# Kernel optimization log

Measured on AMD Instinct MI355X. Metric: run time of the kernel, lower is better.

## Reference

```python
import jax, jax.numpy as jnp
import numpy as np

INPUT_DIM = 1024
CODEBOOK_DIM = 128
CODEBOOK_SIZE = 8192
B, N = 8, 4096


def setup_inputs() -> dict:
    key = jax.random.key(0)
    k1, k2, k3 = jax.random.split(key, 3)
    x = jax.random.normal(k1, (B, N, INPUT_DIM), dtype=jnp.float32)
    # xavier_normal_: std = sqrt(2 / (fan_in + fan_out))
    xavier_std = float(np.sqrt(2.0 / (INPUT_DIM + CODEBOOK_DIM)))
    random_projection = jax.random.normal(k2, (INPUT_DIM, CODEBOOK_DIM), dtype=jnp.float32) * xavier_std
    codebook = jax.random.normal(k3, (CODEBOOK_SIZE, CODEBOOK_DIM), dtype=jnp.float32)
    return {"x": x, "random_projection": random_projection, "codebook": codebook}


def reference(x, random_projection, codebook):
    # random projection: [B, N, D] @ [D, E] -> [B, N, E]
    proj = jnp.einsum("bnd,de->bne", x, random_projection)
    b, n, e = proj.shape
    flat = proj.reshape(b * n, e)  # [BN, E]
    eps = 1e-12  # matches torch F.normalize default eps
    nx = flat / jnp.maximum(jnp.linalg.norm(flat, axis=1, keepdims=True), eps)
    ncb = codebook / jnp.maximum(jnp.linalg.norm(codebook, axis=1, keepdims=True), eps)
    # squared euclidean distances [K, BN]; argmin of d^2 == argmin of cdist
    d2 = (
        jnp.sum(ncb * ncb, axis=1)[:, None]
        + jnp.sum(nx * nx, axis=1)[None, :]
        - 2.0 * (ncb @ nx.T)
    )
    nearest = jnp.argmin(d2, axis=0)  # [BN]
    return nearest.reshape(b, n).astype(jnp.int32)
```

## Files before the change

### kernel.cpp

```cpp
#include <hip/hip_runtime.h>
#include <math.h>
#include <float.h>
#include <limits.h>

#define BN      32768
#define D_IN    1024
#define E_DIM   128
#define CB_N    8192

typedef _Float16 f16x8 __attribute__((ext_vector_type(8)));
typedef _Float16 f16x4 __attribute__((ext_vector_type(4)));
typedef float    f32x4 __attribute__((ext_vector_type(4)));


__global__ __launch_bounds__(256) void pack_all_kernel(
    const float* __restrict__ cb, _Float16* __restrict__ ph,
    _Float16* __restrict__ pl,
    const float* __restrict__ rp, _Float16* __restrict__ rph,
    _Float16* __restrict__ rpl) {
    __shared__ float L[16][129];
    __shared__ float R[32][132];
    const int t = threadIdx.x;
    const int b = blockIdx.x;

    if (b < 512) {
        const int g = b;
        const int c = t >> 4, p = t & 15;
        const float4 v0 = *(const float4*)&cb[(size_t)(g * 16 + c) * E_DIM + p * 8];
        const float4 v1 = *(const float4*)&cb[(size_t)(g * 16 + c) * E_DIM + p * 8 + 4];
        float ss = v0.x * v0.x + v0.y * v0.y + v0.z * v0.z + v0.w * v0.w
                 + v1.x * v1.x + v1.y * v1.y + v1.z * v1.z + v1.w * v1.w;
#pragma unroll
        for (int m = 1; m < 16; m <<= 1) ss += __shfl_xor(ss, m);
        const float inv = 256.0f / fmaxf(sqrtf(ss), 1e-12f);

        L[c][p * 8 + 0] = v0.x * inv; L[c][p * 8 + 1] = v0.y * inv;
        L[c][p * 8 + 2] = v0.z * inv; L[c][p * 8 + 3] = v0.w * inv;
        L[c][p * 8 + 4] = v1.x * inv; L[c][p * 8 + 5] = v1.y * inv;
        L[c][p * 8 + 6] = v1.z * inv; L[c][p * 8 + 7] = v1.w * inv;
        __syncthreads();

        const int kb = t >> 6, lane = t & 63;
        const int quad = (lane >> 4), col = lane & 15;
        f16x8 h, l;
#pragma unroll
        for (int j = 0; j < 8; ++j) {
            const float v = L[col][kb * 32 + quad * 8 + j];
            const _Float16 hv = (_Float16)v;
            h[j] = hv;
            l[j] = (_Float16)(v - (float)hv);
        }
        const size_t off = ((size_t)(g * 4 + kb) * 64 + lane) * 8;
        *(f16x8*)&ph[off] = h;
        *(f16x8*)&pl[off] = l;
    } else {
        const int kb = b - 512;
        const int r = t >> 3, c0 = (t & 7) * 16;
#pragma unroll
        for (int i = 0; i < 4; ++i)
            *(float4*)&R[r][c0 + i * 4] =
                *(const float4*)&rp[(size_t)(kb * 32 + r) * E_DIM + c0 + i * 4];
        __syncthreads();

        const int w = t >> 6, lane = t & 63;
        const int quad = lane >> 4, col = lane & 15;
#pragma unroll
        for (int h2 = 0; h2 < 2; ++h2) {
            const int nt = w * 2 + h2;
            f16x8 hh, ll;
#pragma unroll
            for (int j = 0; j < 8; ++j) {
                const float v = R[quad * 8 + j][nt * 16 + col] * 64.0f;
                const _Float16 hv = (_Float16)v;
                hh[j] = hv;
                ll[j] = (_Float16)(v - (float)hv);
            }
            const size_t off = ((size_t)((kb * 8 + nt) * 64) + lane) * 8;
            *(f16x8*)&rph[off] = hh;
            *(f16x8*)&rpl[off] = ll;
        }
    }
}

#define PPITCH  132

__global__ __launch_bounds__(256, 2) void fused_kernel(
    const float* __restrict__ x,
    const _Float16* __restrict__ rph, const _Float16* __restrict__ rpl,
    const _Float16* __restrict__ ph, const _Float16* __restrict__ pl,
    int* __restrict__ out) {
    __shared__ float    P[64 * PPITCH];
    __shared__ float    ls[4][32];
    __shared__ int      li[4][32];

    const int tid  = threadIdx.x;
    const int lane = tid & 63;
    const int w    = tid >> 6;
    const int quad = lane >> 4, col = lane & 15;
    const int qb   = blockIdx.x * 64;

    const float* xr[4];
#pragma unroll
    for (int mt = 0; mt < 4; ++mt)
        xr[mt] = x + (size_t)(qb + mt * 16 + col) * D_IN + quad * 8;

    f32x4 acc[4][2];
#pragma unroll
    for (int mt = 0; mt < 4; ++mt)
#pragma unroll
        for (int h = 0; h < 2; ++h) acc[mt][h] = (f32x4){0.f, 0.f, 0.f, 0.f};

    float4 pA[4][2];
#pragma unroll
    for (int mt = 0; mt < 4; ++mt) {
        pA[mt][0] = *(const float4*)(xr[mt] + 0);
        pA[mt][1] = *(const float4*)(xr[mt] + 4);
    }
    f16x8 bhc[2], blc[2];
#pragma unroll
    for (int h = 0; h < 2; ++h) {
        const size_t off = ((size_t)(w * 2 + h) * 64 + lane) * 8;
        bhc[h] = *(const f16x8*)&rph[off];
        blc[h] = *(const f16x8*)&rpl[off];
    }

    for (int kb = 0; kb < 32; ++kb) {
        f16x8 ah1[4], al1[4];
#pragma unroll
        for (int mt = 0; mt < 4; ++mt) {
            const float vv[8] = {pA[mt][0].x, pA[mt][0].y, pA[mt][0].z, pA[mt][0].w,
                                 pA[mt][1].x, pA[mt][1].y, pA[mt][1].z, pA[mt][1].w};
            f16x8 hh, ll;
#pragma unroll
            for (int j = 0; j < 8; ++j) {
                const float v = vv[j] * 512.0f;
                const _Float16 hv = (_Float16)v;
                hh[j] = hv;
                ll[j] = (_Float16)(v - (float)hv);
            }
            ah1[mt] = hh;
            al1[mt] = ll;
        }

        if (kb + 1 < 32) {
#pragma unroll
            for (int mt = 0; mt < 4; ++mt) {
                pA[mt][0] = *(const float4*)(xr[mt] + (kb + 1) * 32);
                pA[mt][1] = *(const float4*)(xr[mt] + (kb + 1) * 32 + 4);
            }
        }

        f16x8 bh1[2] = {bhc[0], bhc[1]};
        f16x8 bl1[2] = {blc[0], blc[1]};
        if (kb + 1 < 32) {
#pragma unroll
            for (int h = 0; h < 2; ++h) {
                const size_t off = ((size_t)((kb + 1) * 8 + w * 2 + h) * 64 + lane) * 8;
                bhc[h] = *(const f16x8*)&rph[off];
                blc[h] = *(const f16x8*)&rpl[off];
            }
        }

#pragma unroll
        for (int mt = 0; mt < 4; ++mt)
#pragma unroll
            for (int h = 0; h < 2; ++h)
                acc[mt][h] = __builtin_amdgcn_mfma_f32_16x16x32_f16(ah1[mt], bh1[h], acc[mt][h], 0, 0, 0);
#pragma unroll
        for (int mt = 0; mt < 4; ++mt)
#pragma unroll
            for (int h = 0; h < 2; ++h)
                acc[mt][h] = __builtin_amdgcn_mfma_f32_16x16x32_f16(ah1[mt], bl1[h], acc[mt][h], 0, 0, 0);
#pragma unroll
        for (int mt = 0; mt < 4; ++mt)
#pragma unroll
            for (int h = 0; h < 2; ++h)
                acc[mt][h] = __builtin_amdgcn_mfma_f32_16x16x32_f16(al1[mt], bh1[h], acc[mt][h], 0, 0, 0);
    }

#pragma unroll
    for (int mt = 0; mt < 4; ++mt)
#pragma unroll
        for (int h = 0; h < 2; ++h)
#pragma unroll
            for (int r = 0; r < 4; ++r) {
                const int row = mt * 16 + quad * 4 + r;
                const int cc  = w * 32 + h * 16 + col;
                P[row * PPITCH + cc] = acc[mt][h][r] * (1.0f / 2048.0f);
            }
    __syncthreads();

    const int wq = w >> 1;
    const int wc = w & 1;

    f16x8 ah[2][4], al[2][4];
#pragma unroll
    for (int mt2 = 0; mt2 < 2; ++mt2)
#pragma unroll
        for (int kb = 0; kb < 4; ++kb) {
            const int base = (wq * 32 + mt2 * 16 + col) * PPITCH + kb * 32 + quad * 8;
            const float4 v0 = *(const float4*)&P[base];
            const float4 v1 = *(const float4*)&P[base + 4];
            const float vv[8] = {v0.x, v0.y, v0.z, v0.w, v1.x, v1.y, v1.z, v1.w};
            f16x8 hh, ll;
#pragma unroll
            for (int j = 0; j < 8; ++j) {
                const _Float16 hv = (_Float16)vv[j];
                hh[j] = hv;
                ll[j] = (_Float16)(vv[j] - (float)hv);
            }
            ah[mt2][kb] = hh;
            al[mt2][kb] = ll;
        }

    float bs[8];
    int   bi[8];
#pragma unroll
    for (int s = 0; s < 8; ++s) { bs[s] = -FLT_MAX; bi[s] = 0; }

    const int g0 = wc * 256;

    f16x8 bh[2][4], bl[2][4];
#pragma unroll
    for (int kb = 0; kb < 4; ++kb) {
        const size_t off = ((size_t)(g0 * 4 + kb) * 64 + lane) * 8;
        bh[0][kb] = *(const f16x8*)&ph[off];
        bl[0][kb] = *(const f16x8*)&pl[off];
    }

#pragma unroll 2
    for (int t = 0; t < 256; ++t) {
        const int cur = t & 1, nxt = cur ^ 1;
        if (t + 1 < 256) {
            const int gn = g0 + t + 1;
#pragma unroll
            for (int kb = 0; kb < 4; ++kb) {
                const size_t off = ((size_t)(gn * 4 + kb) * 64 + lane) * 8;
                bh[nxt][kb] = *(const f16x8*)&ph[off];
                bl[nxt][kb] = *(const f16x8*)&pl[off];
            }
        }

        f32x4 sacc[2];
#pragma unroll
        for (int mt2 = 0; mt2 < 2; ++mt2) sacc[mt2] = (f32x4){0.f, 0.f, 0.f, 0.f};

        __builtin_amdgcn_s_setprio(1);
#pragma unroll
        for (int kb = 0; kb < 4; ++kb)
#pragma unroll
            for (int mt2 = 0; mt2 < 2; ++mt2)
                sacc[mt2] = __builtin_amdgcn_mfma_f32_16x16x32_f16(ah[mt2][kb], bh[cur][kb], sacc[mt2], 0, 0, 0);
#pragma unroll
        for (int kb = 0; kb < 4; ++kb)
#pragma unroll
            for (int mt2 = 0; mt2 < 2; ++mt2)
                sacc[mt2] = __builtin_amdgcn_mfma_f32_16x16x32_f16(ah[mt2][kb], bl[cur][kb], sacc[mt2], 0, 0, 0);
#pragma unroll
        for (int kb = 0; kb < 4; ++kb)
#pragma unroll
            for (int mt2 = 0; mt2 < 2; ++mt2)
                sacc[mt2] = __builtin_amdgcn_mfma_f32_16x16x32_f16(al[mt2][kb], bh[cur][kb], sacc[mt2], 0, 0, 0);
        __builtin_amdgcn_s_setprio(0);

        const int code = (g0 + t) * 16 + col;
#pragma unroll
        for (int mt2 = 0; mt2 < 2; ++mt2)
#pragma unroll
            for (int r = 0; r < 4; ++r) {
                const float v = sacc[mt2][r];
                const int s = mt2 * 4 + r;
                if (v > bs[s]) { bs[s] = v; bi[s] = code; }
            }
    }

#pragma unroll
    for (int s = 0; s < 8; ++s) {
#pragma unroll
        for (int m = 1; m < 16; m <<= 1) {
            const float os = __shfl_xor(bs[s], m);
            const int   oi = __shfl_xor(bi[s], m);
            if (os > bs[s] || (os == bs[s] && oi < bi[s])) { bs[s] = os; bi[s] = oi; }
        }
    }

    if (col == 0) {
#pragma unroll
        for (int mt2 = 0; mt2 < 2; ++mt2)
#pragma unroll
            for (int r = 0; r < 4; ++r) {
                ls[w][mt2 * 16 + quad * 4 + r] = bs[mt2 * 4 + r];
                li[w][mt2 * 16 + quad * 4 + r] = bi[mt2 * 4 + r];
            }
    }
    __syncthreads();

    if (tid < 64) {
        const int q   = tid;
        const int wq2 = q >> 5;
        const int q32 = q & 31;
        float s = ls[wq2 * 2 + 0][q32];
        int   i = li[wq2 * 2 + 0][q32];
        const float os = ls[wq2 * 2 + 1][q32];
        if (os > s) { s = os; i = li[wq2 * 2 + 1][q32]; }
        out[qb + q] = i;
    }
}

extern "C" void kernel_launch(void* const* d_in, const int* in_sizes, int n_in,
                              void* d_out, int out_size, void* d_ws, size_t ws_size,
                              hipStream_t stream) {
    const float* x  = (const float*)d_in[0];
    const float* rp = (const float*)d_in[1];
    const float* cb = (const float*)d_in[2];
    int* out = (int*)d_out;

    _Float16* ph  = (_Float16*)d_ws;
    _Float16* pl  = ph  + (size_t)CB_N * E_DIM;
    _Float16* rph = pl  + (size_t)CB_N * E_DIM;
    _Float16* rpl = rph + (size_t)D_IN * E_DIM;

    pack_all_kernel<<<CB_N / 16 + 32, 256, 0, stream>>>(cb, ph, pl, rp, rph, rpl);
    fused_kernel<<<BN / 64, 256, 0, stream>>>(x, rph, rpl, ph, pl, out);
}
```

Before: 392.6 us.

## Stage codebook through double-buffered LDS shared by 8 waves over 128 queries

Doubles the block to 512 threads and 128 queries, and stages codebook hi/lo fragments cooperatively into a double-buffered LDS region that reuses the projection scratch space. Each codebook chunk is now read from global memory once per block and shared by four query-groups, instead of every wave streaming the whole codebook half directly from global memory. In exchange it adds a block-wide barrier per chunk and LDS read traffic, and occupancy may drop because the larger block carries the same register load per wave.

```diff
diff --git a/kernel.cpp b/kernel.cpp
--- a/kernel.cpp
+++ b/kernel.cpp
@@ -83,26 +83,37 @@
 }
 
 #define PPITCH  132
-
-__global__ __launch_bounds__(256, 2) void fused_kernel(
+#define P_BYTES  (128 * PPITCH * 4)
+#define BST_HALF 16384
+#define BST_BUF  32768
+#define NCHUNK   128
+
+__global__ __launch_bounds__(512) void fused_kernel(
     const float* __restrict__ x,
     const _Float16* __restrict__ rph, const _Float16* __restrict__ rpl,
     const _Float16* __restrict__ ph, const _Float16* __restrict__ pl,
     int* __restrict__ out) {
-    __shared__ float    P[64 * PPITCH];
-    __shared__ float    ls[4][32];
-    __shared__ int      li[4][32];
+    __shared__ __align__(16) char SMEM[P_BYTES];
+    __shared__ float ls[8][32];
+    __shared__ int   li[8][32];
 
     const int tid  = threadIdx.x;
     const int lane = tid & 63;
     const int w    = tid >> 6;
     const int quad = lane >> 4, col = lane & 15;
-    const int qb   = blockIdx.x * 64;
+    const int qb   = blockIdx.x * 128;
+
+    float* Pf = (float*)SMEM;
+    char*  Bst = SMEM;
+
+    const int wn  = w & 3;
+    const int wq1 = w >> 2;
+    const int qbw = qb + wq1 * 64;
 
     const float* xr[4];
 #pragma unroll
     for (int mt = 0; mt < 4; ++mt)
-        xr[mt] = x + (size_t)(qb + mt * 16 + col) * D_IN + quad * 8;
+        xr[mt] = x + (size_t)(qbw + mt * 16 + col) * D_IN + quad * 8;
 
     f32x4 acc[4][2];
 #pragma unroll
@@ -119,7 +130,7 @@
     f16x8 bhc[2], blc[2];
 #pragma unroll
     for (int h = 0; h < 2; ++h) {
-        const size_t off = ((size_t)(w * 2 + h) * 64 + lane) * 8;
+        const size_t off = ((size_t)(wn * 2 + h) * 64 + lane) * 8;
         bhc[h] = *(const f16x8*)&rph[off];
         blc[h] = *(const f16x8*)&rpl[off];
     }
@@ -155,7 +166,7 @@
         if (kb + 1 < 32) {
 #pragma unroll
             for (int h = 0; h < 2; ++h) {
-                const size_t off = ((size_t)((kb + 1) * 8 + w * 2 + h) * 64 + lane) * 8;
+                const size_t off = ((size_t)((kb + 1) * 8 + wn * 2 + h) * 64 + lane) * 8;
                 bhc[h] = *(const f16x8*)&rph[off];
                 blc[h] = *(const f16x8*)&rpl[off];
             }
@@ -184,9 +195,9 @@
         for (int h = 0; h < 2; ++h)
 #pragma unroll
             for (int r = 0; r < 4; ++r) {
-                const int row = mt * 16 + quad * 4 + r;
-                const int cc  = w * 32 + h * 16 + col;
-                P[row * PPITCH + cc] = acc[mt][h][r] * (1.0f / 2048.0f);
+                const int row = wq1 * 64 + mt * 16 + quad * 4 + r;
+                const int cc  = wn * 32 + h * 16 + col;
+                Pf[row * PPITCH + cc] = acc[mt][h][r] * (1.0f / 2048.0f);
             }
     __syncthreads();
 
@@ -199,8 +210,8 @@
 #pragma unroll
         for (int kb = 0; kb < 4; ++kb) {
             const int base = (wq * 32 + mt2 * 16 + col) * PPITCH + kb * 32 + quad * 8;
-            const float4 v0 = *(const float4*)&P[base];
-            const float4 v1 = *(const float4*)&P[base + 4];
+            const float4 v0 = *(const float4*)&Pf[base];
+            const float4 v1 = *(const float4*)&Pf[base + 4];
             const float vv[8] = {v0.x, v0.y, v0.z, v0.w, v1.x, v1.y, v1.z, v1.w};
             f16x8 hh, ll;
 #pragma unroll
@@ -212,66 +223,87 @@
             ah[mt2][kb] = hh;
             al[mt2][kb] = ll;
         }
+    __syncthreads();
+
+    const int r_   = w >> 1;
+    const int h2_  = r_ >> 1, sel_ = r_ & 1;
+    const int wh_  = w & 1;
+    const char* sbase   = (const char*)(sel_ ? pl : ph);
+    const size_t goff   = (size_t)h2_ * 1048576 + (size_t)wh_ * 4096 + (size_t)lane * 16;
+    const int    loff   = h2_ * BST_HALF + sel_ * 8192 + wh_ * 4096 + lane * 16;
+
+    float4 stg[4];
+#pragma unroll
+    for (int i = 0; i < 4; ++i)
+        stg[i] = *(const float4*)(sbase + goff + i * 1024);
+#pragma unroll
+    for (int i = 0; i < 4; ++i)
+        *(float4*)(Bst + loff + i * 1024) = stg[i];
+    __syncthreads();
 
     float bs[8];
     int   bi[8];
 #pragma unroll
     for (int s = 0; s < 8; ++s) { bs[s] = -FLT_MAX; bi[s] = 0; }
 
-    const int g0 = wc * 256;
-
-    f16x8 bh[2][4], bl[2][4];
-#pragma unroll
-    for (int kb = 0; kb < 4; ++kb) {
-        const size_t off = ((size_t)(g0 * 4 + kb) * 64 + lane) * 8;
-        bh[0][kb] = *(const f16x8*)&ph[off];
-        bl[0][kb] = *(const f16x8*)&pl[off];
-    }
-
-#pragma unroll 2
-    for (int t = 0; t < 256; ++t) {
-        const int cur = t & 1, nxt = cur ^ 1;
-        if (t + 1 < 256) {
-            const int gn = g0 + t + 1;
+    for (int c = 0; c < NCHUNK; ++c) {
+        const int cur = c & 1;
+        if (c + 1 < NCHUNK) {
+#pragma unroll
+            for (int i = 0; i < 4; ++i)
+                stg[i] = *(const float4*)(sbase + goff + (size_t)(c + 1) * 8192 + i * 1024);
+        }
+
+        const char* bbase = Bst + cur * BST_BUF + wc * BST_HALF;
+#pragma unroll
+        for (int tt = 0; tt < 2; ++tt) {
+            f16x8 bh2[4], bl2[4];
 #pragma unroll
             for (int kb = 0; kb < 4; ++kb) {
-                const size_t off = ((size_t)(gn * 4 + kb) * 64 + lane) * 8;
-                bh[nxt][kb] = *(const f16x8*)&ph[off];
-                bl[nxt][kb] = *(const f16x8*)&pl[off];
-            }
-        }
-
-        f32x4 sacc[2];
-#pragma unroll
-        for (int mt2 = 0; mt2 < 2; ++mt2) sacc[mt2] = (f32x4){0.f, 0.f, 0.f, 0.f};
-
-        __builtin_amdgcn_s_setprio(1);
-#pragma unroll
-        for (int kb = 0; kb < 4; ++kb)
+                bh2[kb] = *(const f16x8*)(bbase + (tt * 4 + kb) * 1024 + lane * 16);
+                bl2[kb] = *(const f16x8*)(bbase + 8192 + (tt * 4 + kb) * 1024 + lane * 16);
+            }
+
+            f32x4 sacc[2];
+#pragma unroll
+            for (int mt2 = 0; mt2 < 2; ++mt2) sacc[mt2] = (f32x4){0.f, 0.f, 0.f, 0.f};
+
+            __builtin_amdgcn_s_setprio(1);
+#pragma unroll
+            for (int kb = 0; kb < 4; ++kb)
+#pragma unroll
+                for (int mt2 = 0; mt2 < 2; ++mt2)
+                    sacc[mt2] = __builtin_amdgcn_mfma_f32_16x16x32_f16(ah[mt2][kb], bh2[kb], sacc[mt2], 0, 0, 0);
+#pragma unroll
+            for (int kb = 0; kb < 4; ++kb)
+#pragma unroll
+                for (int mt2 = 0; mt2 < 2; ++mt2)
+                    sacc[mt2] = __builtin_amdgcn_mfma_f32_16x16x32_f16(ah[mt2][kb], bl2[kb], sacc[mt2], 0, 0, 0);
+#pragma unroll
+            for (int kb = 0; kb < 4; ++kb)
+#pragma unroll
+                for (int mt2 = 0; mt2 < 2; ++mt2)
+                    sacc[mt2] = __builtin_amdgcn_mfma_f32_16x16x32_f16(al[mt2][kb], bh2[kb], sacc[mt2], 0, 0, 0);
+            __builtin_amdgcn_s_setprio(0);
+
+            const int code = wc * 4096 + (c * 2 + tt) * 16 + col;
 #pragma unroll
             for (int mt2 = 0; mt2 < 2; ++mt2)
-                sacc[mt2] = __builtin_amdgcn_mfma_f32_16x16x32_f16(ah[mt2][kb], bh[cur][kb], sacc[mt2], 0, 0, 0);
-#pragma unroll
-        for (int kb = 0; kb < 4; ++kb)
-#pragma unroll
-            for (int mt2 = 0; mt2 < 2; ++mt2)
-                sacc[mt2] = __builtin_amdgcn_mfma_f32_16x16x32_f16(ah[mt2][kb], bl[cur][kb], sacc[mt2], 0, 0, 0);
-#pragma unroll
-        for (int kb = 0; kb < 4; ++kb)
-#pragma unroll
-            for (int mt2 = 0; mt2 < 2; ++mt2)
-                sacc[mt2] = __builtin_amdgcn_mfma_f32_16x16x32_f16(al[mt2][kb], bh[cur][kb], sacc[mt2], 0, 0, 0);
-        __builtin_amdgcn_s_setprio(0);
-
-        const int code = (g0 + t) * 16 + col;
-#pragma unroll
-        for (int mt2 = 0; mt2 < 2; ++mt2)
-#pragma unroll
-            for (int r = 0; r < 4; ++r) {
-                const float v = sacc[mt2][r];
-                const int s = mt2 * 4 + r;
-                if (v > bs[s]) { bs[s] = v; bi[s] = code; }
-            }
+#pragma unroll
+                for (int r = 0; r < 4; ++r) {
+                    const float v = sacc[mt2][r];
+                    const int s = mt2 * 4 + r;
+                    if (v > bs[s]) { bs[s] = v; bi[s] = code; }
+                }
+        }
+
+        if (c + 1 < NCHUNK) {
+            const int nxt = (c + 1) & 1;
+#pragma unroll
+            for (int i = 0; i < 4; ++i)
+                *(float4*)(Bst + nxt * BST_BUF + loff + i * 1024) = stg[i];
+            __syncthreads();
+        }
     }
 
 #pragma unroll
@@ -295,14 +327,14 @@
     }
     __syncthreads();
 
-    if (tid < 64) {
+    if (tid < 128) {
         const int q   = tid;
-        const int wq2 = q >> 5;
+        const int wqf = q >> 5;
         const int q32 = q & 31;
-        float s = ls[wq2 * 2 + 0][q32];
-        int   i = li[wq2 * 2 + 0][q32];
-        const float os = ls[wq2 * 2 + 1][q32];
-        if (os > s) { s = os; i = li[wq2 * 2 + 1][q32]; }
+        float s = ls[wqf * 2 + 0][q32];
+        int   i = li[wqf * 2 + 0][q32];
+        const float os = ls[wqf * 2 + 1][q32];
+        if (os > s) { s = os; i = li[wqf * 2 + 1][q32]; }
         out[qb + q] = i;
     }
 }
@@ -321,5 +353,5 @@
     _Float16* rpl = rph + (size_t)D_IN * E_DIM;
 
     pack_all_kernel<<<CB_N / 16 + 32, 256, 0, stream>>>(cb, ph, pl, rp, rph, rpl);
-    fused_kernel<<<BN / 64, 256, 0, stream>>>(x, rph, rpl, ph, pl, out);
+    fused_kernel<<<BN / 128, 512, 0, stream>>>(x, rph, rpl, ph, pl, out);
 }
```

Measured after the change: 519.1 us. 1.32x slower.

## Halve queries per block and split codebook scan across all four waves

Applied to the files above, without the earlier changes.

Each block now processes 32 query rows instead of 64, doubling the grid. All four waves share the same 32 projected rows and each scans a quarter of the codebook, with a four-way merge at the end. This aims to raise parallelism and occupancy through smaller LDS and accumulator footprints. In exchange, codebook and projection-weight reads are amortised over fewer queries, which increases L2 traffic.

```diff
diff --git a/kernel.cpp b/kernel.cpp
--- a/kernel.cpp
+++ b/kernel.cpp
@@ -82,37 +82,37 @@
     }
 }
 
-#define PPITCH  132
+#define PPITCH   132
 
 __global__ __launch_bounds__(256, 2) void fused_kernel(
     const float* __restrict__ x,
     const _Float16* __restrict__ rph, const _Float16* __restrict__ rpl,
     const _Float16* __restrict__ ph, const _Float16* __restrict__ pl,
     int* __restrict__ out) {
-    __shared__ float    P[64 * PPITCH];
-    __shared__ float    ls[4][32];
-    __shared__ int      li[4][32];
+    __shared__ float P[32 * PPITCH];
+    __shared__ float ls[4][32];
+    __shared__ int   li[4][32];
 
     const int tid  = threadIdx.x;
     const int lane = tid & 63;
     const int w    = tid >> 6;
     const int quad = lane >> 4, col = lane & 15;
-    const int qb   = blockIdx.x * 64;
-
-    const float* xr[4];
-#pragma unroll
-    for (int mt = 0; mt < 4; ++mt)
+    const int qb   = blockIdx.x * 32;
+
+    const float* xr[2];
+#pragma unroll
+    for (int mt = 0; mt < 2; ++mt)
         xr[mt] = x + (size_t)(qb + mt * 16 + col) * D_IN + quad * 8;
 
-    f32x4 acc[4][2];
-#pragma unroll
-    for (int mt = 0; mt < 4; ++mt)
+    f32x4 acc[2][2];
+#pragma unroll
+    for (int mt = 0; mt < 2; ++mt)
 #pragma unroll
         for (int h = 0; h < 2; ++h) acc[mt][h] = (f32x4){0.f, 0.f, 0.f, 0.f};
 
-    float4 pA[4][2];
-#pragma unroll
-    for (int mt = 0; mt < 4; ++mt) {
+    float4 pA[2][2];
+#pragma unroll
+    for (int mt = 0; mt < 2; ++mt) {
         pA[mt][0] = *(const float4*)(xr[mt] + 0);
         pA[mt][1] = *(const float4*)(xr[mt] + 4);
     }
@@ -125,9 +125,9 @@
     }
 
     for (int kb = 0; kb < 32; ++kb) {
-        f16x8 ah1[4], al1[4];
-#pragma unroll
-        for (int mt = 0; mt < 4; ++mt) {
+        f16x8 ah1[2], al1[2];
+#pragma unroll
+        for (int mt = 0; mt < 2; ++mt) {
             const float vv[8] = {pA[mt][0].x, pA[mt][0].y, pA[mt][0].z, pA[mt][0].w,
                                  pA[mt][1].x, pA[mt][1].y, pA[mt][1].z, pA[mt][1].w};
             f16x8 hh, ll;
@@ -144,7 +144,7 @@
 
         if (kb + 1 < 32) {
 #pragma unroll
-            for (int mt = 0; mt < 4; ++mt) {
+            for (int mt = 0; mt < 2; ++mt) {
                 pA[mt][0] = *(const float4*)(xr[mt] + (kb + 1) * 32);
                 pA[mt][1] = *(const float4*)(xr[mt] + (kb + 1) * 32 + 4);
             }
@@ -162,24 +162,24 @@
         }
 
 #pragma unroll
-        for (int mt = 0; mt < 4; ++mt)
+        for (int mt = 0; mt < 2; ++mt)
 #pragma unroll
             for (int h = 0; h < 2; ++h)
                 acc[mt][h] = __builtin_amdgcn_mfma_f32_16x16x32_f16(ah1[mt], bh1[h], acc[mt][h], 0, 0, 0);
 #pragma unroll
-        for (int mt = 0; mt < 4; ++mt)
+        for (int mt = 0; mt < 2; ++mt)
 #pragma unroll
             for (int h = 0; h < 2; ++h)
                 acc[mt][h] = __builtin_amdgcn_mfma_f32_16x16x32_f16(ah1[mt], bl1[h], acc[mt][h], 0, 0, 0);
 #pragma unroll
-        for (int mt = 0; mt < 4; ++mt)
+        for (int mt = 0; mt < 2; ++mt)
 #pragma unroll
             for (int h = 0; h < 2; ++h)
                 acc[mt][h] = __builtin_amdgcn_mfma_f32_16x16x32_f16(al1[mt], bh1[h], acc[mt][h], 0, 0, 0);
     }
 
 #pragma unroll
-    for (int mt = 0; mt < 4; ++mt)
+    for (int mt = 0; mt < 2; ++mt)
 #pragma unroll
         for (int h = 0; h < 2; ++h)
 #pragma unroll
@@ -190,15 +190,12 @@
             }
     __syncthreads();
 
-    const int wq = w >> 1;
-    const int wc = w & 1;
-
     f16x8 ah[2][4], al[2][4];
 #pragma unroll
     for (int mt2 = 0; mt2 < 2; ++mt2)
 #pragma unroll
         for (int kb = 0; kb < 4; ++kb) {
-            const int base = (wq * 32 + mt2 * 16 + col) * PPITCH + kb * 32 + quad * 8;
+            const int base = (mt2 * 16 + col) * PPITCH + kb * 32 + quad * 8;
             const float4 v0 = *(const float4*)&P[base];
             const float4 v1 = *(const float4*)&P[base + 4];
             const float vv[8] = {v0.x, v0.y, v0.z, v0.w, v1.x, v1.y, v1.z, v1.w};
@@ -218,7 +215,7 @@
 #pragma unroll
     for (int s = 0; s < 8; ++s) { bs[s] = -FLT_MAX; bi[s] = 0; }
 
-    const int g0 = wc * 256;
+    const int g0 = w * 128;
 
     f16x8 bh[2][4], bl[2][4];
 #pragma unroll
@@ -229,9 +226,9 @@
     }
 
 #pragma unroll 2
-    for (int t = 0; t < 256; ++t) {
+    for (int t = 0; t < 128; ++t) {
         const int cur = t & 1, nxt = cur ^ 1;
-        if (t + 1 < 256) {
+        if (t + 1 < 128) {
             const int gn = g0 + t + 1;
 #pragma unroll
             for (int kb = 0; kb < 4; ++kb) {
@@ -241,37 +238,36 @@
             }
         }
 
-        f32x4 sacc[2];
-#pragma unroll
-        for (int mt2 = 0; mt2 < 2; ++mt2) sacc[mt2] = (f32x4){0.f, 0.f, 0.f, 0.f};
+        f32x4 s0 = (f32x4){0.f, 0.f, 0.f, 0.f};
+        f32x4 s1 = (f32x4){0.f, 0.f, 0.f, 0.f};
 
         __builtin_amdgcn_s_setprio(1);
 #pragma unroll
-        for (int kb = 0; kb < 4; ++kb)
-#pragma unroll
-            for (int mt2 = 0; mt2 < 2; ++mt2)
-                sacc[mt2] = __builtin_amdgcn_mfma_f32_16x16x32_f16(ah[mt2][kb], bh[cur][kb], sacc[mt2], 0, 0, 0);
-#pragma unroll
-        for (int kb = 0; kb < 4; ++kb)
-#pragma unroll
-            for (int mt2 = 0; mt2 < 2; ++mt2)
-                sacc[mt2] = __builtin_amdgcn_mfma_f32_16x16x32_f16(ah[mt2][kb], bl[cur][kb], sacc[mt2], 0, 0, 0);
-#pragma unroll
-        for (int kb = 0; kb < 4; ++kb)
-#pragma unroll
-            for (int mt2 = 0; mt2 < 2; ++mt2)
-                sacc[mt2] = __builtin_amdgcn_mfma_f32_16x16x32_f16(al[mt2][kb], bh[cur][kb], sacc[mt2], 0, 0, 0);
+        for (int kb = 0; kb < 4; ++kb) {
+            s0 = __builtin_amdgcn_mfma_f32_16x16x32_f16(ah[0][kb], bh[cur][kb], s0, 0, 0, 0);
+            s1 = __builtin_amdgcn_mfma_f32_16x16x32_f16(ah[1][kb], bh[cur][kb], s1, 0, 0, 0);
+        }
+#pragma unroll
+        for (int kb = 0; kb < 4; ++kb) {
+            s0 = __builtin_amdgcn_mfma_f32_16x16x32_f16(ah[0][kb], bl[cur][kb], s0, 0, 0, 0);
+            s1 = __builtin_amdgcn_mfma_f32_16x16x32_f16(ah[1][kb], bl[cur][kb], s1, 0, 0, 0);
+        }
+#pragma unroll
+        for (int kb = 0; kb < 4; ++kb) {
+            s0 = __builtin_amdgcn_mfma_f32_16x16x32_f16(al[0][kb], bh[cur][kb], s0, 0, 0, 0);
+            s1 = __builtin_amdgcn_mfma_f32_16x16x32_f16(al[1][kb], bh[cur][kb], s1, 0, 0, 0);
+        }
         __builtin_amdgcn_s_setprio(0);
 
         const int code = (g0 + t) * 16 + col;
 #pragma unroll
-        for (int mt2 = 0; mt2 < 2; ++mt2)
-#pragma unroll
-            for (int r = 0; r < 4; ++r) {
-                const float v = sacc[mt2][r];
-                const int s = mt2 * 4 + r;
-                if (v > bs[s]) { bs[s] = v; bi[s] = code; }
-            }
+        for (int r = 0; r < 4; ++r) {
+            if (s0[r] > bs[r]) { bs[r] = s0[r]; bi[r] = code; }
+        }
+#pragma unroll
+        for (int r = 0; r < 4; ++r) {
+            if (s1[r] > bs[4 + r]) { bs[4 + r] = s1[r]; bi[4 + r] = code; }
+        }
     }
 
 #pragma unroll
@@ -295,15 +291,15 @@
     }
     __syncthreads();
 
-    if (tid < 64) {
-        const int q   = tid;
-        const int wq2 = q >> 5;
-        const int q32 = q & 31;
-        float s = ls[wq2 * 2 + 0][q32];
-        int   i = li[wq2 * 2 + 0][q32];
-        const float os = ls[wq2 * 2 + 1][q32];
-        if (os > s) { s = os; i = li[wq2 * 2 + 1][q32]; }
-        out[qb + q] = i;
+    if (tid < 32) {
+        float s = ls[0][tid];
+        int   i = li[0][tid];
+#pragma unroll
+        for (int ww = 1; ww < 4; ++ww) {
+            const float os = ls[ww][tid];
+            if (os > s) { s = os; i = li[ww][tid]; }
+        }
+        out[qb + tid] = i;
     }
 }
 
@@ -321,5 +317,5 @@
     _Float16* rpl = rph + (size_t)D_IN * E_DIM;
 
     pack_all_kernel<<<CB_N / 16 + 32, 256, 0, stream>>>(cb, ph, pl, rp, rph, rpl);
-    fused_kernel<<<BN / 64, 256, 0, stream>>>(x, rph, rpl, ph, pl, out);
+    fused_kernel<<<BN / 32, 256, 0, stream>>>(x, rph, rpl, ph, pl, out);
 }
```

Measured after the change: 411.2 us. 1.05x slower.

## Split codebook across all four waves, each scanning all 64 queries

Applied to the files above, without the earlier changes.

The codebook scan is repartitioned. Before, each wave covered 32 queries against half of the codebook. Now each wave covers all 64 queries against a quarter of the codebook, so every codebook fragment loaded from global memory feeds twice as many MFMAs, halving per-wave codebook traffic. The cost is more registers held live (A fragments and best-score state double), which may hurt occupancy or cause spills under launch_bounds(256,2). The final reduction now merges four partial results per query instead of two.

```diff
diff --git a/kernel.cpp b/kernel.cpp
--- a/kernel.cpp
+++ b/kernel.cpp
@@ -90,8 +90,8 @@
     const _Float16* __restrict__ ph, const _Float16* __restrict__ pl,
     int* __restrict__ out) {
     __shared__ float    P[64 * PPITCH];
-    __shared__ float    ls[4][32];
-    __shared__ int      li[4][32];
+    __shared__ float    ls[4][64];
+    __shared__ int      li[4][64];
 
     const int tid  = threadIdx.x;
     const int lane = tid & 63;
@@ -190,15 +190,12 @@
             }
     __syncthreads();
 
-    const int wq = w >> 1;
-    const int wc = w & 1;
-
-    f16x8 ah[2][4], al[2][4];
-#pragma unroll
-    for (int mt2 = 0; mt2 < 2; ++mt2)
+    f16x8 ah[4][4], al[4][4];
+#pragma unroll
+    for (int mt = 0; mt < 4; ++mt)
 #pragma unroll
         for (int kb = 0; kb < 4; ++kb) {
-            const int base = (wq * 32 + mt2 * 16 + col) * PPITCH + kb * 32 + quad * 8;
+            const int base = (mt * 16 + col) * PPITCH + kb * 32 + quad * 8;
             const float4 v0 = *(const float4*)&P[base];
             const float4 v1 = *(const float4*)&P[base + 4];
             const float vv[8] = {v0.x, v0.y, v0.z, v0.w, v1.x, v1.y, v1.z, v1.w};
@@ -209,16 +206,16 @@
                 hh[j] = hv;
                 ll[j] = (_Float16)(vv[j] - (float)hv);
             }
-            ah[mt2][kb] = hh;
-            al[mt2][kb] = ll;
-        }
-
-    float bs[8];
-    int   bi[8];
-#pragma unroll
-    for (int s = 0; s < 8; ++s) { bs[s] = -FLT_MAX; bi[s] = 0; }
-
-    const int g0 = wc * 256;
+            ah[mt][kb] = hh;
+            al[mt][kb] = ll;
+        }
+
+    float bs[16];
+    int   bi[16];
+#pragma unroll
+    for (int s = 0; s < 16; ++s) { bs[s] = -FLT_MAX; bi[s] = 0; }
+
+    const int g0 = w * 128;
 
     f16x8 bh[2][4], bl[2][4];
 #pragma unroll
@@ -229,9 +226,9 @@
     }
 
 #pragma unroll 2
-    for (int t = 0; t < 256; ++t) {
+    for (int t = 0; t < 128; ++t) {
         const int cur = t & 1, nxt = cur ^ 1;
-        if (t + 1 < 256) {
+        if (t + 1 < 128) {
             const int gn = g0 + t + 1;
 #pragma unroll
             for (int kb = 0; kb < 4; ++kb) {
@@ -241,41 +238,41 @@
             }
         }
 
-        f32x4 sacc[2];
-#pragma unroll
-        for (int mt2 = 0; mt2 < 2; ++mt2) sacc[mt2] = (f32x4){0.f, 0.f, 0.f, 0.f};
+        f32x4 sacc[4];
+#pragma unroll
+        for (int mt = 0; mt < 4; ++mt) sacc[mt] = (f32x4){0.f, 0.f, 0.f, 0.f};
 
         __builtin_amdgcn_s_setprio(1);
 #pragma unroll
         for (int kb = 0; kb < 4; ++kb)
 #pragma unroll
-            for (int mt2 = 0; mt2 < 2; ++mt2)
-                sacc[mt2] = __builtin_amdgcn_mfma_f32_16x16x32_f16(ah[mt2][kb], bh[cur][kb], sacc[mt2], 0, 0, 0);
+            for (int mt = 0; mt < 4; ++mt)
+                sacc[mt] = __builtin_amdgcn_mfma_f32_16x16x32_f16(ah[mt][kb], bh[cur][kb], sacc[mt], 0, 0, 0);
 #pragma unroll
         for (int kb = 0; kb < 4; ++kb)
 #pragma unroll
-            for (int mt2 = 0; mt2 < 2; ++mt2)
-                sacc[mt2] = __builtin_amdgcn_mfma_f32_16x16x32_f16(ah[mt2][kb], bl[cur][kb], sacc[mt2], 0, 0, 0);
+            for (int mt = 0; mt < 4; ++mt)
+                sacc[mt] = __builtin_amdgcn_mfma_f32_16x16x32_f16(ah[mt][kb], bl[cur][kb], sacc[mt], 0, 0, 0);
 #pragma unroll
         for (int kb = 0; kb < 4; ++kb)
 #pragma unroll
-            for (int mt2 = 0; mt2 < 2; ++mt2)
-                sacc[mt2] = __builtin_amdgcn_mfma_f32_16x16x32_f16(al[mt2][kb], bh[cur][kb], sacc[mt2], 0, 0, 0);
+            for (int mt = 0; mt < 4; ++mt)
+                sacc[mt] = __builtin_amdgcn_mfma_f32_16x16x32_f16(al[mt][kb], bh[cur][kb], sacc[mt], 0, 0, 0);
         __builtin_amdgcn_s_setprio(0);
 
         const int code = (g0 + t) * 16 + col;
 #pragma unroll
-        for (int mt2 = 0; mt2 < 2; ++mt2)
+        for (int mt = 0; mt < 4; ++mt)
 #pragma unroll
             for (int r = 0; r < 4; ++r) {
-                const float v = sacc[mt2][r];
-                const int s = mt2 * 4 + r;
+                const float v = sacc[mt][r];
+                const int s = mt * 4 + r;
                 if (v > bs[s]) { bs[s] = v; bi[s] = code; }
             }
     }
 
 #pragma unroll
-    for (int s = 0; s < 8; ++s) {
+    for (int s = 0; s < 16; ++s) {
 #pragma unroll
         for (int m = 1; m < 16; m <<= 1) {
             const float os = __shfl_xor(bs[s], m);
@@ -286,23 +283,24 @@
 
     if (col == 0) {
 #pragma unroll
-        for (int mt2 = 0; mt2 < 2; ++mt2)
+        for (int mt = 0; mt < 4; ++mt)
 #pragma unroll
             for (int r = 0; r < 4; ++r) {
-                ls[w][mt2 * 16 + quad * 4 + r] = bs[mt2 * 4 + r];
-                li[w][mt2 * 16 + quad * 4 + r] = bi[mt2 * 4 + r];
+                ls[w][mt * 16 + quad * 4 + r] = bs[mt * 4 + r];
+                li[w][mt * 16 + quad * 4 + r] = bi[mt * 4 + r];
             }
     }
     __syncthreads();
 
     if (tid < 64) {
-        const int q   = tid;
-        const int wq2 = q >> 5;
-        const int q32 = q & 31;
-        float s = ls[wq2 * 2 + 0][q32];
-        int   i = li[wq2 * 2 + 0][q32];
-        const float os = ls[wq2 * 2 + 1][q32];
-        if (os > s) { s = os; i = li[wq2 * 2 + 1][q32]; }
+        const int q = tid;
+        float s = ls[0][q];
+        int   i = li[0][q];
+#pragma unroll
+        for (int ww = 1; ww < 4; ++ww) {
+            const float os = ls[ww][q];
+            if (os > s) { s = os; i = li[ww][q]; }
+        }
         out[qb + q] = i;
     }
 }
```

Result: no change. 395.3 us (+0.7%).
